# Kernel optimization log

Measured on AMD Instinct MI355X. Metric: run time of the kernel, lower is better.

## Reference

```python
import jax, jax.numpy as jnp
import numpy as np

B, N, E, H = 2, 2048, 1024, 16
D = E // H  # head dim = 64


def layer_norm(x, gamma, beta, eps=1e-5):
    m = jnp.mean(x, axis=-1, keepdims=True)
    v = jnp.mean(jnp.square(x - m), axis=-1, keepdims=True)
    return (x - m) * jax.lax.rsqrt(v + eps) * gamma + beta


def setup_inputs() -> dict:
    key = jax.random.key(0)
    ks = jax.random.split(key, 9)
    w_scale = 1.0 / np.sqrt(E)
    Q = jax.random.normal(ks[0], (B, N, E), jnp.float32)
    K = jax.random.normal(ks[1], (B, N, E), jnp.float32)
    V = jax.random.normal(ks[2], (B, N, E), jnp.float32)
    # causal mask: True = masked (matches torch masked_fill_ semantics)
    mask = jnp.broadcast_to(jnp.triu(jnp.ones((N, N), bool), k=1)[None, None], (B, 1, N, N))
    Wq = jax.random.normal(ks[3], (E, E), jnp.float32) * w_scale
    Wk = jax.random.normal(ks[4], (E, E), jnp.float32) * w_scale
    Wv = jax.random.normal(ks[5], (E, E), jnp.float32) * w_scale
    bq = jax.random.normal(ks[6], (E,), jnp.float32) * 0.02
    bk = jax.random.normal(ks[7], (E,), jnp.float32) * 0.02
    bv = jax.random.normal(ks[8], (E,), jnp.float32) * 0.02
    gamma = jnp.ones((E,), jnp.float32)
    beta = jnp.zeros((E,), jnp.float32)
    return dict(Q=Q, K=K, V=V, mask=mask, Wq=Wq, bq=bq, Wk=Wk, bk=bk,
                Wv=Wv, bv=bv, gamma=gamma, beta=beta)


def reference(Q, K, V, mask, Wq, bq, Wk, bk, Wv, bv, gamma, beta):
    resid = Q  # cloned_Q residual
    # pre-norm (same LayerNorm applied to all three streams)
    q = layer_norm(Q, gamma, beta) @ Wq + bq  # [B,N,E]
    k = layer_norm(K, gamma, beta) @ Wk + bk
    v = layer_norm(V, gamma, beta) @ Wv + bv
    # split heads -> [B,H,N,D]
    q = q.reshape(B, N, H, D).transpose(0, 2, 1, 3)
    k = k.reshape(B, N, H, D).transpose(0, 2, 1, 3)
    v = v.reshape(B, N, H, D).transpose(0, 2, 1, 3)
    # scores [B,H,N,N], scaled by sqrt(head_dim)
    s = jnp.einsum('bhnd,bhmd->bhnm', q, k) * (D ** -0.5)
    s = jnp.where(mask, -jnp.inf, s)
    p = jax.nn.softmax(s, axis=-1)
    o = jnp.einsum('bhnm,bhmd->bhnd', p, v)
    o = o.transpose(0, 2, 1, 3).reshape(B, N, E)
    return o + resid
```

## Files before the change

kernel.cpp:

```cpp
#include <hip/hip_runtime.h>
#include <hip/hip_bf16.h>

#define B_ 2
#define N_ 2048
#define E_ 1024
#define H_ 16
#define D_ 64
#define M_TOT (B_*N_)

typedef __attribute__((ext_vector_type(8))) short bf16x8;
typedef __attribute__((ext_vector_type(4))) float f32x4;

__device__ __forceinline__ unsigned short f2bf(float f) {
    unsigned int u = __float_as_uint(f);
    u += 0x7fff + ((u >> 16) & 1);
    return (unsigned short)(u >> 16);
}

__device__ __forceinline__ void gload16(const void* g, void* l) {
    __builtin_amdgcn_global_load_lds(
        (const __attribute__((address_space(1))) unsigned int*)g,
        (__attribute__((address_space(3))) unsigned int*)l, 16, 0, 0);
}

__global__ __launch_bounds__(256) void ln_kernel(
    const float* __restrict__ Q, const float* __restrict__ K,
    const float* __restrict__ V, const float* __restrict__ gamma,
    const float* __restrict__ beta, unsigned short* __restrict__ Xn)
{
    const int row = blockIdx.x;
    const int s   = blockIdx.y;
    const float* X = (s == 0) ? Q : (s == 1) ? K : V;
    const int tid = threadIdx.x;
    const float4 x = ((const float4*)(X + (size_t)row * E_))[tid];
    float sum = x.x + x.y + x.z + x.w;
    float sq  = x.x*x.x + x.y*x.y + x.z*x.z + x.w*x.w;
    #pragma unroll
    for (int off = 32; off > 0; off >>= 1) {
        sum += __shfl_down(sum, off);
        sq  += __shfl_down(sq,  off);
    }
    __shared__ float red[8];
    const int wid = tid >> 6;
    if ((tid & 63) == 0) { red[wid] = sum; red[4 + wid] = sq; }
    __syncthreads();
    if (tid == 0) {
        float s0 = red[0] + red[1] + red[2] + red[3];
        float q0 = red[4] + red[5] + red[6] + red[7];
        red[0] = s0 * (1.0f / E_);
        red[4] = q0 * (1.0f / E_);
    }
    __syncthreads();
    const float mean = red[0];
    const float var  = red[4] - mean * mean;
    const float inv  = rsqrtf(var + 1e-5f);
    const float4 g = ((const float4*)gamma)[tid];
    const float4 b = ((const float4*)beta)[tid];
    ushort4 o;
    o.x = f2bf((x.x - mean) * inv * g.x + b.x);
    o.y = f2bf((x.y - mean) * inv * g.y + b.y);
    o.z = f2bf((x.z - mean) * inv * g.z + b.z);
    o.w = f2bf((x.w - mean) * inv * g.w + b.w);
    const int bo = 8 * tid;
    const int bs = (bo & ~127) | ((bo & 127) ^ ((row & 7) << 4));
    char* rowp = (char*)(Xn + (size_t)s * M_TOT * E_ + (size_t)row * E_);
    *(ushort4*)(rowp + bs) = o;
}

__global__ __launch_bounds__(256) void wt_kernel(
    const float* __restrict__ Wq, const float* __restrict__ Wk,
    const float* __restrict__ Wv, unsigned short* __restrict__ Wt)
{
    const int s = blockIdx.z;
    const float* W = (s == 0) ? Wq : (s == 1) ? Wk : Wv;
    __shared__ float tile[32][33];
    const int tx = threadIdx.x, ty = threadIdx.y;
    const int n0 = blockIdx.x * 32, k0 = blockIdx.y * 32;
    #pragma unroll
    for (int i = 0; i < 4; i++)
        tile[ty + 8*i][tx] = W[(size_t)(k0 + ty + 8*i) * E_ + n0 + tx];
    __syncthreads();
    unsigned short* dst = Wt + (size_t)s * E_ * E_;
    #pragma unroll
    for (int i = 0; i < 4; i++) {
        const int n = n0 + ty + 8*i;
        const int bo = 2 * (k0 + tx);
        const int bs = (bo & ~127) | ((bo & 127) ^ ((n & 7) << 4));
        *(unsigned short*)((char*)(dst + (size_t)n * E_) + bs) =
            f2bf(tile[tx][ty + 8*i]);
    }
}

__global__ __launch_bounds__(256, 3) void gemm_kernel(
    const unsigned short* __restrict__ Xn, const unsigned short* __restrict__ Wt,
    const float* __restrict__ bq, const float* __restrict__ bk,
    const float* __restrict__ bv, unsigned short* __restrict__ QKVh)
{
    const int bid = blockIdx.x;
    const int wk  = (bid & 7) * 96 + (bid >> 3);
    const int s   = wk >> 8;
    const int rem = wk & 255;
    const int m0  = (rem >> 3) * 128;
    const int n0  = (rem & 7) * 128;
    const float* bias = (s == 0) ? bq : (s == 1) ? bk : bv;
    const unsigned short* A  = Xn + (size_t)s * M_TOT * E_;
    const unsigned short* Bw = Wt + (size_t)s * E_ * E_;
    unsigned short* out = QKVh + (size_t)s * M_TOT * E_;
    const int tid = threadIdx.x;
    const int lane = tid & 63;
    const int w = tid >> 6;
    const int l15 = lane & 15, lhi = lane >> 4;

    __shared__ unsigned short Al[2][128][64];

    const int srow = lane >> 3;
    const int scol = (lane & 7) * 8;
    const int rx = (l15 & 7) << 4;

    const char* bbase = (const char*)Bw + (size_t)(n0 + w*32 + l15) * (E_ * 2);

    f32x4 acc[8][2];
    #pragma unroll
    for (int m = 0; m < 8; m++)
        #pragma unroll
        for (int n = 0; n < 2; n++)
            acc[m][n] = (f32x4){0.f, 0.f, 0.f, 0.f};

    #define STAGEA(b_, kt_) do {                                             \
        const int k0_ = (kt_) * 64;                                          \
        _Pragma("unroll")                                                    \
        for (int ii = 0; ii < 4; ii++) {                                     \
            const int r_ = w*32 + ii*8;                                      \
            gload16(A + (size_t)(m0 + r_ + srow) * E_ + k0_ + scol,          \
                    &Al[b_][r_][0]);                                         \
        }                                                                    \
    } while (0)

    STAGEA(0, 0);
    for (int kt = 0; kt < 16; kt++) {
        const int buf = kt & 1;
        bf16x8 bfr[2][2];
        #pragma unroll
        for (int ks = 0; ks < 2; ks++)
            #pragma unroll
            for (int n = 0; n < 2; n++)
                bfr[ks][n] = *(const bf16x8*)(bbase + (size_t)n * 16 * (E_ * 2)
                               + kt*128 + ((ks*64 + lhi*16) ^ rx));
        __syncthreads();
        if (kt + 1 < 16) STAGEA(buf ^ 1, kt + 1);
        const char* ab = (const char*)Al[buf];
        #pragma unroll
        for (int ks = 0; ks < 2; ks++) {
            #pragma unroll
            for (int m = 0; m < 8; m++) {
                bf16x8 af = *(const bf16x8*)(ab
                        + (m*16 + l15)*128 + ((ks*64 + lhi*16) ^ rx));
                #pragma unroll
                for (int n = 0; n < 2; n++)
                    acc[m][n] = __builtin_amdgcn_mfma_f32_16x16x32_bf16(
                        af, bfr[ks][n], acc[m][n], 0, 0, 0);
            }
        }
    }
    #undef STAGEA

    const float scale = (s == 0) ? 0.18033688011112042f : 1.0f;
    #pragma unroll
    for (int n = 0; n < 2; n++) {
        const int gn = n0 + w*32 + n*16 + l15;
        const float bv_ = bias[gn];
        const int h = gn >> 6, d = gn & 63;
        #pragma unroll
        for (int m = 0; m < 8; m++) {
            const int gmBase = m0 + m*16 + lhi*4;
            if (s == 2) {
                const int bb2 = gmBase >> 11, nseq = gmBase & 2047;
                ushort4 pk;
                pk.x = f2bf(acc[m][n][0] + bv_);
                pk.y = f2bf(acc[m][n][1] + bv_);
                pk.z = f2bf(acc[m][n][2] + bv_);
                pk.w = f2bf(acc[m][n][3] + bv_);
                *(ushort4*)(out + ((size_t)(bb2*H_ + h) * D_ + d) * N_ + nseq)
                    = pk;
            } else {
                #pragma unroll
                for (int j = 0; j < 4; j++) {
                    const int gm = gmBase + j;
                    const int bb2 = gm >> 11, nseq = gm & 2047;
                    out[((size_t)(bb2*H_ + h) * N_ + nseq) * D_ + d] =
                        f2bf((acc[m][n][j] + bv_) * scale);
                }
            }
        }
    }
}

__global__ __launch_bounds__(512, 4) void attn_kernel(
    const unsigned short* __restrict__ QKVh, const float* __restrict__ Qin,
    float* __restrict__ out)
{
    const int slot = blockIdx.x >> 5;
    const int bh   = blockIdx.x & 31;
    const int tid = threadIdx.x;
    const int lane = tid & 63;
    const int w = tid >> 6;
    const int h = w >> 2;
    const int rg = w & 3;
    const int l15 = lane & 15, lhi = lane >> 4;
    const size_t headOff = (size_t)bh * N_ * D_;
    const unsigned short* qh = QKVh + headOff;
    const unsigned short* kh = QKVh + (size_t)M_TOT * E_ + headOff;
    const unsigned short* vh = QKVh + (size_t)2 * M_TOT * E_ + headOff;

    __shared__ unsigned short Kt[2][64*64];
    __shared__ unsigned short Vt[2][64*64];
    __shared__ unsigned short Pl[8][16*64];
    __shared__ float Ml[4][16];

    const int sr  = (tid >> 3) & 63;
    const int sce = (tid & 7) * 8;
    const int wofs = sr * 128 + (((tid & 7) * 16) ^ ((sr & 7) << 4));
    const int rxor = (l15 & 7) << 4;

    const int bb = bh >> 4, hh = bh & 15;

    {
        uint4 ka  = *(const uint4*)(kh + (size_t)sr * D_ + sce);
        uint4 kb2 = *(const uint4*)(kh + (size_t)(64 + sr) * D_ + sce);
        uint4 va  = *(const uint4*)(vh + (size_t)sr * N_ + sce);
        uint4 vb2 = *(const uint4*)(vh + (size_t)sr * N_ + 64 + sce);
        *(uint4*)((char*)Kt[0] + wofs) = ka;
        *(uint4*)((char*)Kt[1] + wofs) = kb2;
        *(uint4*)((char*)Vt[0] + wofs) = va;
        *(uint4*)((char*)Vt[1] + wofs) = vb2;
    }

    #pragma unroll 1
    for (int pass = 0; pass < 2; pass++) {
        const int g  = pass ? slot : 31 - slot;
        const int q0 = g * 64;
        const int wlo = q0 + rg * 16;
        const int S = (g + 2) >> 1;

        bf16x8 qf[2];
        #pragma unroll
        for (int ks = 0; ks < 2; ks++)
            qf[ks] = *(const bf16x8*)(qh + (size_t)(wlo + l15) * D_
                                          + ks*32 + lhi*8);

        f32x4 o[4];
        #pragma unroll
        for (int n = 0; n < 4; n++) o[n] = (f32x4){0.f, 0.f, 0.f, 0.f};
        float l_i = 0.f;

        #pragma unroll 1
        for (int s = 0; s < S; s++) {
            __syncthreads();
            uint4 nka, nkb, nva, nvb;
            bool pre = true; int kvn;
            if (s + 1 < S)       kvn = (s + 1) * 128;
            else if (pass == 0)  kvn = 0;
            else                 { pre = false; kvn = 0; }
            if (pre) {
                nka = *(const uint4*)(kh + (size_t)(kvn + sr) * D_ + sce);
                nkb = *(const uint4*)(kh + (size_t)(kvn + 64 + sr) * D_ + sce);
                nva = *(const uint4*)(vh + (size_t)sr * N_ + kvn + sce);
                nvb = *(const uint4*)(vh + (size_t)sr * N_ + kvn + 64 + sce);
            }
            const int t = 2*s + h;
            if (t <= g) {
                const int kv0 = t * 64;
                const char* kbb = (const char*)Kt[t & 1];
                const char* vbb = (const char*)Vt[t & 1];
                f32x4 sfr[4];
                #pragma unroll
                for (int n = 0; n < 4; n++) sfr[n] = (f32x4){0.f,0.f,0.f,0.f};
                #pragma unroll
                for (int ks = 0; ks < 2; ks++) {
                    bf16x8 kb[4];
                    #pragma unroll
                    for (int n = 0; n < 4; n++)
                        kb[n] = *(const bf16x8*)(kbb + (n*16 + l15)*128
                                                     + ((ks*64 + lhi*16) ^ rxor));
                    __builtin_amdgcn_s_setprio(1);
                    #pragma unroll
                    for (int n = 0; n < 4; n++)
                        sfr[n] = __builtin_amdgcn_mfma_f32_16x16x32_bf16(
                            kb[n], qf[ks], sfr[n], 0, 0, 0);
                    __builtin_amdgcn_s_setprio(0);
                }
                const int qr = wlo + l15;
                if (t == g) {
                    #pragma unroll
                    for (int n = 0; n < 4; n++)
                        #pragma unroll
                        for (int j = 0; j < 4; j++) {
                            int kvc = kv0 + n*16 + lhi*4 + j;
                            sfr[n][j] = (kvc > qr) ? -1e30f : sfr[n][j];
                        }
                }
                float rs = 0.f;
                #pragma unroll
                for (int n = 0; n < 4; n++)
                    #pragma unroll
                    for (int j = 0; j < 4; j++) {
                        float p = exp2f(sfr[n][j]);
                        sfr[n][j] = p;
                        rs += p;
                    }
                rs += __shfl_xor(rs, 16);
                rs += __shfl_xor(rs, 32);
                l_i += rs;
                char* pw = (char*)Pl[w];
                #pragma unroll
                for (int n = 0; n < 4; n++) {
                    unsigned int u0 = __float_as_uint(sfr[n][0]) + 0x8000u;
                    unsigned int u1 = __float_as_uint(sfr[n][1]) + 0x8000u;
                    unsigned int u2 = __float_as_uint(sfr[n][2]) + 0x8000u;
                    unsigned int u3 = __float_as_uint(sfr[n][3]) + 0x8000u;
                    uint2 pk;
                    pk.x = __builtin_amdgcn_perm(u1, u0, 0x07060302u);
                    pk.y = __builtin_amdgcn_perm(u3, u2, 0x07060302u);
                    *(uint2*)(pw + l15*128 + ((n*32 + lhi*8) ^ rxor)) = pk;
                }
                #pragma unroll
                for (int ks = 0; ks < 2; ks++) {
                    bf16x8 pb = *(const bf16x8*)(pw + l15*128
                                                 + ((ks*64 + lhi*16) ^ rxor));
                    bf16x8 vbr[4];
                    #pragma unroll
                    for (int n = 0; n < 4; n++)
                        vbr[n] = *(const bf16x8*)(vbb + (n*16 + l15)*128
                                                      + ((ks*64 + lhi*16) ^ rxor));
                    __builtin_amdgcn_s_setprio(1);
                    #pragma unroll
                    for (int n = 0; n < 4; n++)
                        o[n] = __builtin_amdgcn_mfma_f32_16x16x32_bf16(
                            vbr[n], pb, o[n], 0, 0, 0);
                    __builtin_amdgcn_s_setprio(0);
                }
            }
            __syncthreads();
            if (pre) {
                *(uint4*)((char*)Kt[0] + wofs) = nka;
                *(uint4*)((char*)Kt[1] + wofs) = nkb;
                *(uint4*)((char*)Vt[0] + wofs) = nva;
                *(uint4*)((char*)Vt[1] + wofs) = nvb;
            }
        }
        __syncthreads();
        if (h == 1) {
            char* ob = (char*)Pl + rg * 4096;
            #pragma unroll
            for (int n = 0; n < 4; n++)
                *(f32x4*)(ob + l15*256 + ((n*64 + lhi*16) ^ rxor)) = o[n];
            if (lhi == 0) Ml[rg][l15] = l_i;
        }
        __syncthreads();
        if (h == 0) {
            const float linv = 1.0f / (l_i + Ml[rg][l15]);
            const char* ob = (const char*)Pl + rg * 4096;
            const int qr = wlo + l15;
            #pragma unroll
            for (int n = 0; n < 4; n++) {
                f32x4 o1 = *(const f32x4*)(ob + l15*256 + ((n*64 + lhi*16) ^ rxor));
                const int d0 = n*16 + lhi*4;
                size_t idx = ((size_t)(bb * N_ + qr)) * E_ + hh * D_ + d0;
                float4 r = *(const float4*)(Qin + idx);
                float4 ov;
                ov.x = (o[n][0] + o1[0]) * linv + r.x;
                ov.y = (o[n][1] + o1[1]) * linv + r.y;
                ov.z = (o[n][2] + o1[2]) * linv + r.z;
                ov.w = (o[n][3] + o1[3]) * linv + r.w;
                *(float4*)(out + idx) = ov;
            }
        }
    }
}

extern "C" void kernel_launch(void* const* d_in, const int* in_sizes, int n_in,
                              void* d_out, int out_size, void* d_ws, size_t ws_size,
                              hipStream_t stream) {
    const float* Q     = (const float*)d_in[0];
    const float* K     = (const float*)d_in[1];
    const float* V     = (const float*)d_in[2];
    const float* Wq    = (const float*)d_in[4];
    const float* bq    = (const float*)d_in[5];
    const float* Wk    = (const float*)d_in[6];
    const float* bk    = (const float*)d_in[7];
    const float* Wv    = (const float*)d_in[8];
    const float* bv    = (const float*)d_in[9];
    const float* gamma = (const float*)d_in[10];
    const float* beta  = (const float*)d_in[11];
    float* out = (float*)d_out;

    char* ws = (char*)d_ws;
    unsigned short* Xn   = (unsigned short*)ws;
    unsigned short* Wt   = (unsigned short*)(ws + 25165824);
    unsigned short* QKVh = (unsigned short*)(ws + 31457280);

    ln_kernel  <<<dim3(4096, 3),   256,        0, stream>>>(Q, K, V, gamma, beta, Xn);
    wt_kernel  <<<dim3(32, 32, 3), dim3(32,8), 0, stream>>>(Wq, Wk, Wv, Wt);
    gemm_kernel<<<dim3(768),       256,        0, stream>>>(Xn, Wt, bq, bk, bv, QKVh);
    attn_kernel<<<dim3(512),       512,        0, stream>>>(QKVh, Q, out);
}
```

Measured before the change: 91.85 us.

## Restructure attention into single-wave blocks loading K/V directly from global

The attention kernel goes from 512-thread blocks that share K/V tiles through LDS, with two-pass causal load balancing, to 2048 single-wave blocks. Each block handles 32 query rows and reads K/V fragments straight from global memory into registers, prefetching the next K tile. The row sum is now computed with an MFMA against a ones vector instead of shuffles, and block-wide syncs and the cross-wave reduction are gone. The cost is that K/V reuse across waves through LDS is lost, which raises global/L2 traffic, and blocks are scheduled longest-first to balance the causal workload.

```diff
diff --git a/kernel.cpp b/kernel.cpp
--- a/kernel.cpp
+++ b/kernel.cpp
@@ -195,185 +195,159 @@
     }
 }
 
-__global__ __launch_bounds__(512, 4) void attn_kernel(
+__global__ __launch_bounds__(64, 2) void attn_kernel(
     const unsigned short* __restrict__ QKVh, const float* __restrict__ Qin,
     float* __restrict__ out)
 {
-    const int slot = blockIdx.x >> 5;
-    const int bh   = blockIdx.x & 31;
-    const int tid = threadIdx.x;
-    const int lane = tid & 63;
-    const int w = tid >> 6;
-    const int h = w >> 2;
-    const int rg = w & 3;
+    const int bid = blockIdx.x;
+    const int bh  = bid & 31;
+    const int qg  = 63 - (bid >> 5);
+    const int q0  = qg * 32;
+    const int nt  = (qg >> 1) + 1;
+    const int tdiag = nt - 1;
+    const int lane = threadIdx.x;
     const int l15 = lane & 15, lhi = lane >> 4;
+    const int rxor = (l15 & 7) << 4;
+
     const size_t headOff = (size_t)bh * N_ * D_;
-    const unsigned short* qh = QKVh + headOff;
+    const unsigned short* qp = QKVh + headOff;
     const unsigned short* kh = QKVh + (size_t)M_TOT * E_ + headOff;
     const unsigned short* vh = QKVh + (size_t)2 * M_TOT * E_ + headOff;
 
-    __shared__ unsigned short Kt[2][64*64];
-    __shared__ unsigned short Vt[2][64*64];
-    __shared__ unsigned short Pl[8][16*64];
-    __shared__ float Ml[4][16];
-
-    const int sr  = (tid >> 3) & 63;
-    const int sce = (tid & 7) * 8;
-    const int wofs = sr * 128 + (((tid & 7) * 16) ^ ((sr & 7) << 4));
-    const int rxor = (l15 & 7) << 4;
-
-    const int bb = bh >> 4, hh = bh & 15;
-
-    {
-        uint4 ka  = *(const uint4*)(kh + (size_t)sr * D_ + sce);
-        uint4 kb2 = *(const uint4*)(kh + (size_t)(64 + sr) * D_ + sce);
-        uint4 va  = *(const uint4*)(vh + (size_t)sr * N_ + sce);
-        uint4 vb2 = *(const uint4*)(vh + (size_t)sr * N_ + 64 + sce);
-        *(uint4*)((char*)Kt[0] + wofs) = ka;
-        *(uint4*)((char*)Kt[1] + wofs) = kb2;
-        *(uint4*)((char*)Vt[0] + wofs) = va;
-        *(uint4*)((char*)Vt[1] + wofs) = vb2;
-    }
+    __shared__ unsigned short Pl[32 * 64];
+
+    bf16x8 qf[2][2];
+    #pragma unroll
+    for (int qh = 0; qh < 2; qh++)
+        #pragma unroll
+        for (int ks = 0; ks < 2; ks++)
+            qf[qh][ks] = *(const bf16x8*)(qp
+                + (size_t)(q0 + qh*16 + l15) * D_ + ks*32 + lhi*8);
+
+    const char* kbase = (const char*)kh + l15*128 + lhi*16;
+    const char* vbase = (const char*)vh + l15*4096 + lhi*16;
+
+    const f32x4 fz = {0.f, 0.f, 0.f, 0.f};
+    f32x4 o[2][4], ol[2];
+    #pragma unroll
+    for (int qh = 0; qh < 2; qh++) {
+        ol[qh] = fz;
+        #pragma unroll
+        for (int n = 0; n < 4; n++) o[qh][n] = fz;
+    }
+    bf16x8 ones;
+    #pragma unroll
+    for (int i = 0; i < 8; i++) ones[i] = (short)0x3F80;
+
+    bf16x8 kb[2][4];
+    #pragma unroll
+    for (int ks = 0; ks < 2; ks++)
+        #pragma unroll
+        for (int n = 0; n < 4; n++)
+            kb[ks][n] = *(const bf16x8*)(kbase + n*2048 + ks*64);
+
+    char* pw = (char*)Pl;
 
     #pragma unroll 1
-    for (int pass = 0; pass < 2; pass++) {
-        const int g  = pass ? slot : 31 - slot;
-        const int q0 = g * 64;
-        const int wlo = q0 + rg * 16;
-        const int S = (g + 2) >> 1;
-
-        bf16x8 qf[2];
+    for (int t = 0; t < nt; t++) {
+        const char* vt = vbase + t*128;
+        bf16x8 vb[2][4];
         #pragma unroll
         for (int ks = 0; ks < 2; ks++)
-            qf[ks] = *(const bf16x8*)(qh + (size_t)(wlo + l15) * D_
-                                          + ks*32 + lhi*8);
-
-        f32x4 o[4];
-        #pragma unroll
-        for (int n = 0; n < 4; n++) o[n] = (f32x4){0.f, 0.f, 0.f, 0.f};
-        float l_i = 0.f;
-
-        #pragma unroll 1
-        for (int s = 0; s < S; s++) {
-            __syncthreads();
-            uint4 nka, nkb, nva, nvb;
-            bool pre = true; int kvn;
-            if (s + 1 < S)       kvn = (s + 1) * 128;
-            else if (pass == 0)  kvn = 0;
-            else                 { pre = false; kvn = 0; }
-            if (pre) {
-                nka = *(const uint4*)(kh + (size_t)(kvn + sr) * D_ + sce);
-                nkb = *(const uint4*)(kh + (size_t)(kvn + 64 + sr) * D_ + sce);
-                nva = *(const uint4*)(vh + (size_t)sr * N_ + kvn + sce);
-                nvb = *(const uint4*)(vh + (size_t)sr * N_ + kvn + 64 + sce);
-            }
-            const int t = 2*s + h;
-            if (t <= g) {
-                const int kv0 = t * 64;
-                const char* kbb = (const char*)Kt[t & 1];
-                const char* vbb = (const char*)Vt[t & 1];
-                f32x4 sfr[4];
-                #pragma unroll
-                for (int n = 0; n < 4; n++) sfr[n] = (f32x4){0.f,0.f,0.f,0.f};
-                #pragma unroll
-                for (int ks = 0; ks < 2; ks++) {
-                    bf16x8 kb[4];
-                    #pragma unroll
-                    for (int n = 0; n < 4; n++)
-                        kb[n] = *(const bf16x8*)(kbb + (n*16 + l15)*128
-                                                     + ((ks*64 + lhi*16) ^ rxor));
-                    __builtin_amdgcn_s_setprio(1);
-                    #pragma unroll
-                    for (int n = 0; n < 4; n++)
-                        sfr[n] = __builtin_amdgcn_mfma_f32_16x16x32_bf16(
-                            kb[n], qf[ks], sfr[n], 0, 0, 0);
-                    __builtin_amdgcn_s_setprio(0);
-                }
-                const int qr = wlo + l15;
-                if (t == g) {
-                    #pragma unroll
-                    for (int n = 0; n < 4; n++)
-                        #pragma unroll
-                        for (int j = 0; j < 4; j++) {
-                            int kvc = kv0 + n*16 + lhi*4 + j;
-                            sfr[n][j] = (kvc > qr) ? -1e30f : sfr[n][j];
-                        }
-                }
-                float rs = 0.f;
+            #pragma unroll
+            for (int n = 0; n < 4; n++)
+                vb[ks][n] = *(const bf16x8*)(vt + n*65536 + ks*64);
+
+        f32x4 sf[2][4];
+        __builtin_amdgcn_s_setprio(1);
+        #pragma unroll
+        for (int qh = 0; qh < 2; qh++)
+            #pragma unroll
+            for (int n = 0; n < 4; n++)
+                sf[qh][n] = __builtin_amdgcn_mfma_f32_16x16x32_bf16(
+                    kb[1][n], qf[qh][1],
+                    __builtin_amdgcn_mfma_f32_16x16x32_bf16(
+                        kb[0][n], qf[qh][0], fz, 0, 0, 0), 0, 0, 0);
+        __builtin_amdgcn_s_setprio(0);
+
+        if (t == tdiag) {
+            #pragma unroll
+            for (int qh = 0; qh < 2; qh++) {
+                const int qr = q0 + qh*16 + l15;
                 #pragma unroll
                 for (int n = 0; n < 4; n++)
                     #pragma unroll
                     for (int j = 0; j < 4; j++) {
-                        float p = exp2f(sfr[n][j]);
-                        sfr[n][j] = p;
-                        rs += p;
+                        const int kvc = t*64 + n*16 + lhi*4 + j;
+                        sf[qh][n][j] = (kvc > qr) ? -1e30f : sf[qh][n][j];
                     }
-                rs += __shfl_xor(rs, 16);
-                rs += __shfl_xor(rs, 32);
-                l_i += rs;
-                char* pw = (char*)Pl[w];
+            }
+        }
+
+        #pragma unroll
+        for (int qh = 0; qh < 2; qh++) {
+            const int prow = (qh*16 + l15) * 128;
+            #pragma unroll
+            for (int n = 0; n < 4; n++) {
+                unsigned int u0 = __float_as_uint(exp2f(sf[qh][n][0])) + 0x8000u;
+                unsigned int u1 = __float_as_uint(exp2f(sf[qh][n][1])) + 0x8000u;
+                unsigned int u2 = __float_as_uint(exp2f(sf[qh][n][2])) + 0x8000u;
+                unsigned int u3 = __float_as_uint(exp2f(sf[qh][n][3])) + 0x8000u;
+                uint2 pk;
+                pk.x = __builtin_amdgcn_perm(u1, u0, 0x07060302u);
+                pk.y = __builtin_amdgcn_perm(u3, u2, 0x07060302u);
+                *(uint2*)(pw + prow + ((n*32 + lhi*8) ^ rxor)) = pk;
+            }
+        }
+
+        if (t + 1 < nt) {
+            const char* kt = kbase + (size_t)(t + 1) * 8192;
+            #pragma unroll
+            for (int ks = 0; ks < 2; ks++)
                 #pragma unroll
-                for (int n = 0; n < 4; n++) {
-                    unsigned int u0 = __float_as_uint(sfr[n][0]) + 0x8000u;
-                    unsigned int u1 = __float_as_uint(sfr[n][1]) + 0x8000u;
-                    unsigned int u2 = __float_as_uint(sfr[n][2]) + 0x8000u;
-                    unsigned int u3 = __float_as_uint(sfr[n][3]) + 0x8000u;
-                    uint2 pk;
-                    pk.x = __builtin_amdgcn_perm(u1, u0, 0x07060302u);
-                    pk.y = __builtin_amdgcn_perm(u3, u2, 0x07060302u);
-                    *(uint2*)(pw + l15*128 + ((n*32 + lhi*8) ^ rxor)) = pk;
-                }
-                #pragma unroll
-                for (int ks = 0; ks < 2; ks++) {
-                    bf16x8 pb = *(const bf16x8*)(pw + l15*128
-                                                 + ((ks*64 + lhi*16) ^ rxor));
-                    bf16x8 vbr[4];
-                    #pragma unroll
-                    for (int n = 0; n < 4; n++)
-                        vbr[n] = *(const bf16x8*)(vbb + (n*16 + l15)*128
-                                                      + ((ks*64 + lhi*16) ^ rxor));
-                    __builtin_amdgcn_s_setprio(1);
-                    #pragma unroll
-                    for (int n = 0; n < 4; n++)
-                        o[n] = __builtin_amdgcn_mfma_f32_16x16x32_bf16(
-                            vbr[n], pb, o[n], 0, 0, 0);
-                    __builtin_amdgcn_s_setprio(0);
-                }
-            }
-            __syncthreads();
-            if (pre) {
-                *(uint4*)((char*)Kt[0] + wofs) = nka;
-                *(uint4*)((char*)Kt[1] + wofs) = nkb;
-                *(uint4*)((char*)Vt[0] + wofs) = nva;
-                *(uint4*)((char*)Vt[1] + wofs) = nvb;
-            }
-        }
-        __syncthreads();
-        if (h == 1) {
-            char* ob = (char*)Pl + rg * 4096;
-            #pragma unroll
-            for (int n = 0; n < 4; n++)
-                *(f32x4*)(ob + l15*256 + ((n*64 + lhi*16) ^ rxor)) = o[n];
-            if (lhi == 0) Ml[rg][l15] = l_i;
-        }
-        __syncthreads();
-        if (h == 0) {
-            const float linv = 1.0f / (l_i + Ml[rg][l15]);
-            const char* ob = (const char*)Pl + rg * 4096;
-            const int qr = wlo + l15;
+                for (int n = 0; n < 4; n++)
+                    kb[ks][n] = *(const bf16x8*)(kt + n*2048 + ks*64);
+        }
+
+        #pragma unroll
+        for (int ks = 0; ks < 2; ks++) {
+            bf16x8 pb[2];
+            #pragma unroll
+            for (int qh = 0; qh < 2; qh++)
+                pb[qh] = *(const bf16x8*)(pw + (qh*16 + l15)*128
+                                             + ((ks*64 + lhi*16) ^ rxor));
+            __builtin_amdgcn_s_setprio(1);
             #pragma unroll
             for (int n = 0; n < 4; n++) {
-                f32x4 o1 = *(const f32x4*)(ob + l15*256 + ((n*64 + lhi*16) ^ rxor));
-                const int d0 = n*16 + lhi*4;
-                size_t idx = ((size_t)(bb * N_ + qr)) * E_ + hh * D_ + d0;
-                float4 r = *(const float4*)(Qin + idx);
-                float4 ov;
-                ov.x = (o[n][0] + o1[0]) * linv + r.x;
-                ov.y = (o[n][1] + o1[1]) * linv + r.y;
-                ov.z = (o[n][2] + o1[2]) * linv + r.z;
-                ov.w = (o[n][3] + o1[3]) * linv + r.w;
-                *(float4*)(out + idx) = ov;
-            }
+                o[0][n] = __builtin_amdgcn_mfma_f32_16x16x32_bf16(
+                    vb[ks][n], pb[0], o[0][n], 0, 0, 0);
+                o[1][n] = __builtin_amdgcn_mfma_f32_16x16x32_bf16(
+                    vb[ks][n], pb[1], o[1][n], 0, 0, 0);
+            }
+            ol[0] = __builtin_amdgcn_mfma_f32_16x16x32_bf16(
+                ones, pb[0], ol[0], 0, 0, 0);
+            ol[1] = __builtin_amdgcn_mfma_f32_16x16x32_bf16(
+                ones, pb[1], ol[1], 0, 0, 0);
+            __builtin_amdgcn_s_setprio(0);
+        }
+    }
+
+    const int bb = bh >> 4, hh = bh & 15;
+    #pragma unroll
+    for (int qh = 0; qh < 2; qh++) {
+        const float linv = 1.0f / ol[qh][0];
+        const int qr = q0 + qh*16 + l15;
+        #pragma unroll
+        for (int n = 0; n < 4; n++) {
+            const int d0 = n*16 + lhi*4;
+            const size_t idx = ((size_t)(bb * N_ + qr)) * E_ + hh * D_ + d0;
+            const float4 r = *(const float4*)(Qin + idx);
+            float4 ov;
+            ov.x = o[qh][n][0] * linv + r.x;
+            ov.y = o[qh][n][1] * linv + r.y;
+            ov.z = o[qh][n][2] * linv + r.z;
+            ov.w = o[qh][n][3] * linv + r.w;
+            *(float4*)(out + idx) = ov;
         }
     }
 }
@@ -402,5 +376,5 @@
     ln_kernel  <<<dim3(4096, 3),   256,        0, stream>>>(Q, K, V, gamma, beta, Xn);
     wt_kernel  <<<dim3(32, 32, 3), dim3(32,8), 0, stream>>>(Wq, Wk, Wv, Wt);
     gemm_kernel<<<dim3(768),       256,        0, stream>>>(Xn, Wt, bq, bk, bv, QKVh);
-    attn_kernel<<<dim3(512),       512,        0, stream>>>(QKVh, Q, out);
-}
+    attn_kernel<<<dim3(2048),      64,         0, stream>>>(QKVh, Q, out);
+}
```

Result: slower. 125.3 us (+36.5%).

## Split paired attention passes into separate blocks; compute row sums via MFMA

Applied to the files above, without the earlier changes.

Each attention block previously handled two query tiles (g and 31-g) in sequence, for load balance. Now the grid is doubled so each block handles a single query tile, with the heaviest tiles launched first. Separately, the softmax denominator is no longer built from per-element exp sums and cross-lane shuffles. It comes from an extra MFMA that multiplies the bf16 P tile by a ones vector, so the normaliser matches the rounded P used in the PV product. The change adds one MFMA per k-step and gives up the cross-pass K/V prefetch, in exchange for more parallel blocks and less VALU and shuffle work.

```diff
diff --git a/kernel.cpp b/kernel.cpp
--- a/kernel.cpp
+++ b/kernel.cpp
@@ -199,8 +199,12 @@
     const unsigned short* __restrict__ QKVh, const float* __restrict__ Qin,
     float* __restrict__ out)
 {
-    const int slot = blockIdx.x >> 5;
-    const int bh   = blockIdx.x & 31;
+    const int bid  = blockIdx.x;
+    const int slot = bid >> 5;
+    const int bh   = bid & 31;
+    const int g    = 31 - slot;
+    const int q0   = g * 64;
+    const int S    = (g + 2) >> 1;
     const int tid = threadIdx.x;
     const int lane = tid & 63;
     const int w = tid >> 6;
@@ -223,6 +227,7 @@
     const int rxor = (l15 & 7) << 4;
 
     const int bb = bh >> 4, hh = bh & 15;
+    const int wlo = q0 + rg * 16;
 
     {
         uint4 ka  = *(const uint4*)(kh + (size_t)sr * D_ + sce);
@@ -235,145 +240,131 @@
         *(uint4*)((char*)Vt[1] + wofs) = vb2;
     }
 
+    bf16x8 qf[2];
+    #pragma unroll
+    for (int ks = 0; ks < 2; ks++)
+        qf[ks] = *(const bf16x8*)(qh + (size_t)(wlo + l15) * D_
+                                      + ks*32 + lhi*8);
+
+    const f32x4 fz = {0.f, 0.f, 0.f, 0.f};
+    f32x4 o[4], ol;
+    #pragma unroll
+    for (int n = 0; n < 4; n++) o[n] = fz;
+    ol = fz;
+    bf16x8 ones;
+    #pragma unroll
+    for (int i = 0; i < 8; i++) ones[i] = (short)0x3F80;
+
     #pragma unroll 1
-    for (int pass = 0; pass < 2; pass++) {
-        const int g  = pass ? slot : 31 - slot;
-        const int q0 = g * 64;
-        const int wlo = q0 + rg * 16;
-        const int S = (g + 2) >> 1;
-
-        bf16x8 qf[2];
-        #pragma unroll
-        for (int ks = 0; ks < 2; ks++)
-            qf[ks] = *(const bf16x8*)(qh + (size_t)(wlo + l15) * D_
-                                          + ks*32 + lhi*8);
-
-        f32x4 o[4];
-        #pragma unroll
-        for (int n = 0; n < 4; n++) o[n] = (f32x4){0.f, 0.f, 0.f, 0.f};
-        float l_i = 0.f;
-
-        #pragma unroll 1
-        for (int s = 0; s < S; s++) {
-            __syncthreads();
-            uint4 nka, nkb, nva, nvb;
-            bool pre = true; int kvn;
-            if (s + 1 < S)       kvn = (s + 1) * 128;
-            else if (pass == 0)  kvn = 0;
-            else                 { pre = false; kvn = 0; }
-            if (pre) {
-                nka = *(const uint4*)(kh + (size_t)(kvn + sr) * D_ + sce);
-                nkb = *(const uint4*)(kh + (size_t)(kvn + 64 + sr) * D_ + sce);
-                nva = *(const uint4*)(vh + (size_t)sr * N_ + kvn + sce);
-                nvb = *(const uint4*)(vh + (size_t)sr * N_ + kvn + 64 + sce);
-            }
-            const int t = 2*s + h;
-            if (t <= g) {
-                const int kv0 = t * 64;
-                const char* kbb = (const char*)Kt[t & 1];
-                const char* vbb = (const char*)Vt[t & 1];
-                f32x4 sfr[4];
-                #pragma unroll
-                for (int n = 0; n < 4; n++) sfr[n] = (f32x4){0.f,0.f,0.f,0.f};
-                #pragma unroll
-                for (int ks = 0; ks < 2; ks++) {
-                    bf16x8 kb[4];
-                    #pragma unroll
-                    for (int n = 0; n < 4; n++)
-                        kb[n] = *(const bf16x8*)(kbb + (n*16 + l15)*128
-                                                     + ((ks*64 + lhi*16) ^ rxor));
-                    __builtin_amdgcn_s_setprio(1);
-                    #pragma unroll
-                    for (int n = 0; n < 4; n++)
-                        sfr[n] = __builtin_amdgcn_mfma_f32_16x16x32_bf16(
-                            kb[n], qf[ks], sfr[n], 0, 0, 0);
-                    __builtin_amdgcn_s_setprio(0);
-                }
-                const int qr = wlo + l15;
-                if (t == g) {
-                    #pragma unroll
-                    for (int n = 0; n < 4; n++)
-                        #pragma unroll
-                        for (int j = 0; j < 4; j++) {
-                            int kvc = kv0 + n*16 + lhi*4 + j;
-                            sfr[n][j] = (kvc > qr) ? -1e30f : sfr[n][j];
-                        }
-                }
-                float rs = 0.f;
+    for (int s = 0; s < S; s++) {
+        __syncthreads();
+        uint4 nka, nkb, nva, nvb;
+        const bool pre = (s + 1 < S);
+        if (pre) {
+            const int kvn = (s + 1) * 128;
+            nka = *(const uint4*)(kh + (size_t)(kvn + sr) * D_ + sce);
+            nkb = *(const uint4*)(kh + (size_t)(kvn + 64 + sr) * D_ + sce);
+            nva = *(const uint4*)(vh + (size_t)sr * N_ + kvn + sce);
+            nvb = *(const uint4*)(vh + (size_t)sr * N_ + kvn + 64 + sce);
+        }
+        const int t = 2*s + h;
+        if (t <= g) {
+            const int kv0 = t * 64;
+            const char* kbb = (const char*)Kt[t & 1];
+            const char* vbb = (const char*)Vt[t & 1];
+            f32x4 sfr[4];
+            #pragma unroll
+            for (int n = 0; n < 4; n++) sfr[n] = fz;
+            #pragma unroll
+            for (int ks = 0; ks < 2; ks++) {
+                bf16x8 kb[4];
+                #pragma unroll
+                for (int n = 0; n < 4; n++)
+                    kb[n] = *(const bf16x8*)(kbb + (n*16 + l15)*128
+                                                 + ((ks*64 + lhi*16) ^ rxor));
+                __builtin_amdgcn_s_setprio(1);
+                #pragma unroll
+                for (int n = 0; n < 4; n++)
+                    sfr[n] = __builtin_amdgcn_mfma_f32_16x16x32_bf16(
+                        kb[n], qf[ks], sfr[n], 0, 0, 0);
+                __builtin_amdgcn_s_setprio(0);
+            }
+            const int qr = wlo + l15;
+            if (t == g) {
                 #pragma unroll
                 for (int n = 0; n < 4; n++)
                     #pragma unroll
                     for (int j = 0; j < 4; j++) {
-                        float p = exp2f(sfr[n][j]);
-                        sfr[n][j] = p;
-                        rs += p;
+                        int kvc = kv0 + n*16 + lhi*4 + j;
+                        sfr[n][j] = (kvc > qr) ? -1e30f : sfr[n][j];
                     }
-                rs += __shfl_xor(rs, 16);
-                rs += __shfl_xor(rs, 32);
-                l_i += rs;
-                char* pw = (char*)Pl[w];
-                #pragma unroll
-                for (int n = 0; n < 4; n++) {
-                    unsigned int u0 = __float_as_uint(sfr[n][0]) + 0x8000u;
-                    unsigned int u1 = __float_as_uint(sfr[n][1]) + 0x8000u;
-                    unsigned int u2 = __float_as_uint(sfr[n][2]) + 0x8000u;
-                    unsigned int u3 = __float_as_uint(sfr[n][3]) + 0x8000u;
-                    uint2 pk;
-                    pk.x = __builtin_amdgcn_perm(u1, u0, 0x07060302u);
-                    pk.y = __builtin_amdgcn_perm(u3, u2, 0x07060302u);
-                    *(uint2*)(pw + l15*128 + ((n*32 + lhi*8) ^ rxor)) = pk;
-                }
-                #pragma unroll
-                for (int ks = 0; ks < 2; ks++) {
-                    bf16x8 pb = *(const bf16x8*)(pw + l15*128
-                                                 + ((ks*64 + lhi*16) ^ rxor));
-                    bf16x8 vbr[4];
-                    #pragma unroll
-                    for (int n = 0; n < 4; n++)
-                        vbr[n] = *(const bf16x8*)(vbb + (n*16 + l15)*128
-                                                      + ((ks*64 + lhi*16) ^ rxor));
-                    __builtin_amdgcn_s_setprio(1);
-                    #pragma unroll
-                    for (int n = 0; n < 4; n++)
-                        o[n] = __builtin_amdgcn_mfma_f32_16x16x32_bf16(
-                            vbr[n], pb, o[n], 0, 0, 0);
-                    __builtin_amdgcn_s_setprio(0);
-                }
-            }
-            __syncthreads();
-            if (pre) {
-                *(uint4*)((char*)Kt[0] + wofs) = nka;
-                *(uint4*)((char*)Kt[1] + wofs) = nkb;
-                *(uint4*)((char*)Vt[0] + wofs) = nva;
-                *(uint4*)((char*)Vt[1] + wofs) = nvb;
+            }
+            char* pw = (char*)Pl[w];
+            #pragma unroll
+            for (int n = 0; n < 4; n++) {
+                unsigned int u0 = __float_as_uint(exp2f(sfr[n][0])) + 0x8000u;
+                unsigned int u1 = __float_as_uint(exp2f(sfr[n][1])) + 0x8000u;
+                unsigned int u2 = __float_as_uint(exp2f(sfr[n][2])) + 0x8000u;
+                unsigned int u3 = __float_as_uint(exp2f(sfr[n][3])) + 0x8000u;
+                uint2 pk;
+                pk.x = __builtin_amdgcn_perm(u1, u0, 0x07060302u);
+                pk.y = __builtin_amdgcn_perm(u3, u2, 0x07060302u);
+                *(uint2*)(pw + l15*128 + ((n*32 + lhi*8) ^ rxor)) = pk;
+            }
+            #pragma unroll
+            for (int ks = 0; ks < 2; ks++) {
+                bf16x8 pb = *(const bf16x8*)(pw + l15*128
+                                             + ((ks*64 + lhi*16) ^ rxor));
+                bf16x8 vbr[4];
+                #pragma unroll
+                for (int n = 0; n < 4; n++)
+                    vbr[n] = *(const bf16x8*)(vbb + (n*16 + l15)*128
+                                                  + ((ks*64 + lhi*16) ^ rxor));
+                __builtin_amdgcn_s_setprio(1);
+                #pragma unroll
+                for (int n = 0; n < 4; n++)
+                    o[n] = __builtin_amdgcn_mfma_f32_16x16x32_bf16(
+                        vbr[n], pb, o[n], 0, 0, 0);
+                ol = __builtin_amdgcn_mfma_f32_16x16x32_bf16(
+                    ones, pb, ol, 0, 0, 0);
+                __builtin_amdgcn_s_setprio(0);
             }
         }
         __syncthreads();
-        if (h == 1) {
-            char* ob = (char*)Pl + rg * 4096;
-            #pragma unroll
-            for (int n = 0; n < 4; n++)
-                *(f32x4*)(ob + l15*256 + ((n*64 + lhi*16) ^ rxor)) = o[n];
-            if (lhi == 0) Ml[rg][l15] = l_i;
-        }
-        __syncthreads();
-        if (h == 0) {
-            const float linv = 1.0f / (l_i + Ml[rg][l15]);
-            const char* ob = (const char*)Pl + rg * 4096;
-            const int qr = wlo + l15;
-            #pragma unroll
-            for (int n = 0; n < 4; n++) {
-                f32x4 o1 = *(const f32x4*)(ob + l15*256 + ((n*64 + lhi*16) ^ rxor));
-                const int d0 = n*16 + lhi*4;
-                size_t idx = ((size_t)(bb * N_ + qr)) * E_ + hh * D_ + d0;
-                float4 r = *(const float4*)(Qin + idx);
-                float4 ov;
-                ov.x = (o[n][0] + o1[0]) * linv + r.x;
-                ov.y = (o[n][1] + o1[1]) * linv + r.y;
-                ov.z = (o[n][2] + o1[2]) * linv + r.z;
-                ov.w = (o[n][3] + o1[3]) * linv + r.w;
-                *(float4*)(out + idx) = ov;
-            }
+        if (pre) {
+            *(uint4*)((char*)Kt[0] + wofs) = nka;
+            *(uint4*)((char*)Kt[1] + wofs) = nkb;
+            *(uint4*)((char*)Vt[0] + wofs) = nva;
+            *(uint4*)((char*)Vt[1] + wofs) = nvb;
+        }
+    }
+
+    const float l_i = ol[0];
+    __syncthreads();
+    if (h == 1) {
+        char* ob = (char*)Pl + rg * 4096;
+        #pragma unroll
+        for (int n = 0; n < 4; n++)
+            *(f32x4*)(ob + l15*256 + ((n*64 + lhi*16) ^ rxor)) = o[n];
+        if (lhi == 0) Ml[rg][l15] = l_i;
+    }
+    __syncthreads();
+    if (h == 0) {
+        const float linv = 1.0f / (l_i + Ml[rg][l15]);
+        const char* ob = (const char*)Pl + rg * 4096;
+        const int qr = wlo + l15;
+        #pragma unroll
+        for (int n = 0; n < 4; n++) {
+            f32x4 o1 = *(const f32x4*)(ob + l15*256 + ((n*64 + lhi*16) ^ rxor));
+            const int d0 = n*16 + lhi*4;
+            size_t idx = ((size_t)(bb * N_ + qr)) * E_ + hh * D_ + d0;
+            float4 r = *(const float4*)(Qin + idx);
+            float4 ov;
+            ov.x = (o[n][0] + o1[0]) * linv + r.x;
+            ov.y = (o[n][1] + o1[1]) * linv + r.y;
+            ov.z = (o[n][2] + o1[2]) * linv + r.z;
+            ov.w = (o[n][3] + o1[3]) * linv + r.w;
+            *(float4*)(out + idx) = ov;
         }
     }
 }
@@ -402,5 +393,5 @@
     ln_kernel  <<<dim3(4096, 3),   256,        0, stream>>>(Q, K, V, gamma, beta, Xn);
     wt_kernel  <<<dim3(32, 32, 3), dim3(32,8), 0, stream>>>(Wq, Wk, Wv, Wt);
     gemm_kernel<<<dim3(768),       256,        0, stream>>>(Xn, Wt, bq, bk, bv, QKVh);
-    attn_kernel<<<dim3(512),       512,        0, stream>>>(QKVh, Q, out);
-}
+    attn_kernel<<<dim3(1024),      512,        0, stream>>>(QKVh, Q, out);
+}
```

Result: no change. 93.40 us (+1.7%).
